# Kernel tuning notes

Hardware: AMD Instinct MI355X
Metric: run time of the kernel (lower is better)

## Reference

```python
import jax, jax.numpy as jnp
import numpy as np

TEMP = 0.1
EPS = 1e-9  # torch CosineSimilarity eps


def setup_inputs() -> dict:
    key = jax.random.key(0)
    k1, k2 = jax.random.split(key)
    h = jax.random.normal(k1, (16384, 2048), dtype=jnp.float32)
    W = jax.random.normal(k2, (512, 2048), dtype=jnp.float32) * (1.0 / np.sqrt(2048))
    return {"h": h, "W": W}


def reference(h, W):
    # process_reps: h already 2D -> identity. Split into anchor / context halves.
    B = h.shape[0] // 2
    wz = h[:B] @ W.T      # [B, low_rank_dim]
    wc = h[B:] @ W.T      # [B, low_rank_dim]

    # CosineSimilarity(dim=-1, eps=1e-9): dot / max(||z||*||c||, eps), pairwise BxB
    nz = jnp.linalg.norm(wz, axis=-1)  # [B]
    nc = jnp.linalg.norm(wc, axis=-1)  # [B]
    sim = (wz @ wc.T) / jnp.maximum(nz[:, None] * nc[None, :], EPS)  # [B, B]
    sim = sim / TEMP

    sim_mean = sim.mean()
    sim_pos = jnp.diagonal(sim).mean()
    logprob = -jax.nn.log_softmax(sim, axis=1)
    loss = jnp.diagonal(logprob).mean()
    # matches loss_dict entries: {'loss', 'loss_pos', 'loss_neg'}
    return jnp.stack([loss, sim_pos, sim_mean])
```

## Files before the change

kernel.cpp:

```cpp
#include <hip/hip_runtime.h>


typedef __attribute__((ext_vector_type(8))) short bf16x8;
typedef __attribute__((ext_vector_type(4))) float floatx4;
typedef unsigned char uchar;

__device__ __forceinline__ unsigned short f2bf(float f) {
    union { float f; unsigned u; } v; v.f = f;
    unsigned r = (v.u + 0x7FFFu + ((v.u >> 16) & 1u)) >> 16;
    return (unsigned short)r;
}

__device__ __forceinline__ void async_copy16(const void* g, void* l) {
    __builtin_amdgcn_global_load_lds(
        (const __attribute__((address_space(1))) void*)g,
        (__attribute__((address_space(3))) void*)l,
        16, 0, 0);
}

__global__ __launch_bounds__(256) void cast_fp8_kernel(
    const float* __restrict__ src, uchar* __restrict__ dst, int n, float scale)
{
    const int i = (blockIdx.x * 256 + threadIdx.x) * 8;
    if (i + 7 < n) {
        float4 a = *reinterpret_cast<const float4*>(src + i);
        float4 b = *reinterpret_cast<const float4*>(src + i + 4);
        const int p01 = __builtin_amdgcn_cvt_pk_fp8_f32(a.x * scale, a.y * scale, 0, 0);
        const int p23 = __builtin_amdgcn_cvt_pk_fp8_f32(a.z * scale, a.w * scale, 0, 0);
        const int p45 = __builtin_amdgcn_cvt_pk_fp8_f32(b.x * scale, b.y * scale, 0, 0);
        const int p67 = __builtin_amdgcn_cvt_pk_fp8_f32(b.z * scale, b.w * scale, 0, 0);
        int2 w;
        w.x = (p01 & 0xffff) | (p23 << 16);
        w.y = (p45 & 0xffff) | (p67 << 16);
        *reinterpret_cast<int2*>(dst + i) = w;
    }
}

__device__ __forceinline__ size_t fl_off(int row_g, int col_g) {
    const int g = row_g >> 4, r15 = row_g & 15;
    const int c = col_g >> 5, q = (col_g >> 3) & 3, b = col_g & 7;
    return ((size_t)g * 16 + c) * 512 + (size_t)(q * 16 + r15) * 8 + b;
}

__global__ __launch_bounds__(256) void g1_main(
    const uchar* __restrict__ h8, const uchar* __restrict__ W8,
    uchar* __restrict__ Z8F, float* __restrict__ norm2)
{
    __shared__ __align__(16) uchar As[128 * 64];
    __shared__ __align__(16) uchar Bs[128 * 64];

    const int bn = blockIdx.x;
    const int bm = blockIdx.y;
    const int t = threadIdx.x;
    const int wave = t >> 6, lane = t & 63;
    const int wm = wave & 1, wn = wave >> 1;
    const int quad = lane >> 4, l15 = lane & 15;

    floatx4 acc[4][4];
    #pragma unroll
    for (int i = 0; i < 4; i++)
        #pragma unroll
        for (int j = 0; j < 4; j++) acc[i][j] = {0.f, 0.f, 0.f, 0.f};

    const int srow0 = wave * 32 + (lane >> 2);
    const int srow1 = srow0 + 16;
    const int p = lane & 3;
    const int sw0 = (p ^ ((srow0 >> 1) & 3)) << 4;
    const int sw1 = (p ^ ((srow1 >> 1) & 3)) << 4;
    const uchar* gA0 = h8 + (size_t)(bm * 128 + srow0) * 2048 + sw0;
    const uchar* gA1 = h8 + (size_t)(bm * 128 + srow1) * 2048 + sw1;
    const uchar* gB0 = W8 + (size_t)(bn * 128 + srow0) * 2048 + sw0;
    const uchar* gB1 = W8 + (size_t)(bn * 128 + srow1) * 2048 + sw1;
    uchar* lA0 = &As[(wave * 32 +  0) * 64];
    uchar* lA1 = &As[(wave * 32 + 16) * 64];
    uchar* lB0 = &Bs[(wave * 32 +  0) * 64];
    uchar* lB1 = &Bs[(wave * 32 + 16) * 64];

    for (int k0 = 0; k0 < 2048; k0 += 64) {
        async_copy16(gA0 + k0, lA0);
        async_copy16(gA1 + k0, lA1);
        async_copy16(gB0 + k0, lB0);
        async_copy16(gB1 + k0, lB1);
        __syncthreads();
        #pragma unroll
        for (int ch = 0; ch < 2; ch++) {
            const int s = ch * 2 + (quad >> 1);
            const int sub = (quad & 1) * 8;
            long a[4], b[4];
            #pragma unroll
            for (int i = 0; i < 4; i++) {
                const int row = wm * 64 + i * 16 + l15;
                a[i] = *reinterpret_cast<const long*>(
                    &As[row * 64 + ((s ^ ((row >> 1) & 3)) << 4) + sub]);
            }
            #pragma unroll
            for (int j = 0; j < 4; j++) {
                const int row = wn * 64 + j * 16 + l15;
                b[j] = *reinterpret_cast<const long*>(
                    &Bs[row * 64 + ((s ^ ((row >> 1) & 3)) << 4) + sub]);
            }
            #pragma unroll
            for (int i = 0; i < 4; i++)
                #pragma unroll
                for (int j = 0; j < 4; j++)
                    acc[i][j] = __builtin_amdgcn_mfma_f32_16x16x32_fp8_fp8(
                        a[i], b[j], acc[i][j], 0, 0, 0);
        }
        __syncthreads();
    }

    #pragma unroll
    for (int i = 0; i < 4; i++) {
        #pragma unroll
        for (int r = 0; r < 4; r++) {
            const int row_g = bm * 128 + wm * 64 + i * 16 + quad * 4 + r;
            const int pk01 = __builtin_amdgcn_cvt_pk_fp8_f32(acc[i][0][r], acc[i][1][r], 0, 0);
            const int pk23 = __builtin_amdgcn_cvt_pk_fp8_f32(acc[i][2][r], acc[i][3][r], 0, 0);
            const uchar q8[4] = { (uchar)(pk01 & 0xff), (uchar)((pk01 >> 8) & 0xff),
                                  (uchar)(pk23 & 0xff), (uchar)((pk23 >> 8) & 0xff) };
            #pragma unroll
            for (int j = 0; j < 4; j++) {
                const int col_g = bn * 128 + wn * 64 + j * 16 + l15;
                Z8F[fl_off(row_g, col_g)] = q8[j];
            }
            const float q0 = __builtin_amdgcn_cvt_f32_fp8(pk01, 0);
            const float q1 = __builtin_amdgcn_cvt_f32_fp8(pk01, 1);
            const float q2 = __builtin_amdgcn_cvt_f32_fp8(pk23, 0);
            const float q3 = __builtin_amdgcn_cvt_f32_fp8(pk23, 1);
            float pw = q0 * q0 + q1 * q1 + q2 * q2 + q3 * q3;
            pw += __shfl_xor(pw, 1, 16);
            pw += __shfl_xor(pw, 2, 16);
            pw += __shfl_xor(pw, 4, 16);
            pw += __shfl_xor(pw, 8, 16);
            if (l15 == 0) atomicAdd(&norm2[row_g], pw);
        }
    }
}

__global__ __launch_bounds__(256) void g1_slow(
    const float* __restrict__ h, const float* __restrict__ W,
    uchar* __restrict__ Z8F, float* __restrict__ norm2)
{
    __shared__ __align__(16) unsigned short As[128][40];
    __shared__ __align__(16) unsigned short Bs[128][40];

    const int bn = blockIdx.x, bm = blockIdx.y;
    const int t = threadIdx.x;
    const int wave = t >> 6, lane = t & 63;
    const int wm = wave & 1, wn = wave >> 1;
    const int quad = lane >> 4, l15 = lane & 15;

    floatx4 acc[4][4];
    #pragma unroll
    for (int i = 0; i < 4; i++)
        #pragma unroll
        for (int j = 0; j < 4; j++) acc[i][j] = {0.f, 0.f, 0.f, 0.f};

    const int lrow = t >> 1, lhalf = t & 1;
    const float* ga = h + (size_t)(bm * 128 + lrow) * 2048 + lhalf * 16;
    const float* gb = W + (size_t)(bn * 128 + lrow) * 2048 + lhalf * 16;

    for (int k0 = 0; k0 < 2048; k0 += 32) {
        #pragma unroll
        for (int c = 0; c < 4; c++) {
            const float4 va = *reinterpret_cast<const float4*>(ga + k0 + c * 4);
            const float4 vb = *reinterpret_cast<const float4*>(gb + k0 + c * 4);
            ushort4 ua = make_ushort4(f2bf(va.x), f2bf(va.y), f2bf(va.z), f2bf(va.w));
            ushort4 ub = make_ushort4(f2bf(vb.x), f2bf(vb.y), f2bf(vb.z), f2bf(vb.w));
            *reinterpret_cast<ushort4*>(&As[lrow][lhalf * 16 + c * 4]) = ua;
            *reinterpret_cast<ushort4*>(&Bs[lrow][lhalf * 16 + c * 4]) = ub;
        }
        __syncthreads();
        bf16x8 af[4], bfr[4];
        #pragma unroll
        for (int i = 0; i < 4; i++)
            af[i] = *reinterpret_cast<const bf16x8*>(&As[wm * 64 + i * 16 + l15][quad * 8]);
        #pragma unroll
        for (int j = 0; j < 4; j++)
            bfr[j] = *reinterpret_cast<const bf16x8*>(&Bs[wn * 64 + j * 16 + l15][quad * 8]);
        #pragma unroll
        for (int i = 0; i < 4; i++)
            #pragma unroll
            for (int j = 0; j < 4; j++)
                acc[i][j] = __builtin_amdgcn_mfma_f32_16x16x32_bf16(af[i], bfr[j], acc[i][j], 0, 0, 0);
        __syncthreads();
    }

    #pragma unroll
    for (int i = 0; i < 4; i++) {
        #pragma unroll
        for (int r = 0; r < 4; r++) {
            const int row_g = bm * 128 + wm * 64 + i * 16 + quad * 4 + r;
            const int pk01 = __builtin_amdgcn_cvt_pk_fp8_f32(acc[i][0][r], acc[i][1][r], 0, 0);
            const int pk23 = __builtin_amdgcn_cvt_pk_fp8_f32(acc[i][2][r], acc[i][3][r], 0, 0);
            const uchar q8[4] = { (uchar)(pk01 & 0xff), (uchar)((pk01 >> 8) & 0xff),
                                  (uchar)(pk23 & 0xff), (uchar)((pk23 >> 8) & 0xff) };
            #pragma unroll
            for (int j = 0; j < 4; j++) {
                const int col_g = bn * 128 + wn * 64 + j * 16 + l15;
                Z8F[fl_off(row_g, col_g)] = q8[j];
            }
            const float q0 = __builtin_amdgcn_cvt_f32_fp8(pk01, 0);
            const float q1 = __builtin_amdgcn_cvt_f32_fp8(pk01, 1);
            const float q2 = __builtin_amdgcn_cvt_f32_fp8(pk23, 0);
            const float q3 = __builtin_amdgcn_cvt_f32_fp8(pk23, 1);
            float pw = q0 * q0 + q1 * q1 + q2 * q2 + q3 * q3;
            pw += __shfl_xor(pw, 1, 16);
            pw += __shfl_xor(pw, 2, 16);
            pw += __shfl_xor(pw, 4, 16);
            pw += __shfl_xor(pw, 8, 16);
            if (l15 == 0) atomicAdd(&norm2[row_g], pw);
        }
    }
}

__global__ __launch_bounds__(256, 2) void g2_main(
    const uchar* __restrict__ Z8F, const float* __restrict__ norm2,
    float* __restrict__ rowse, float* __restrict__ bsum, float* __restrict__ bdiag)
{
    __shared__ float lds_red[2][128][18];
    __shared__ float red[8];

    const int bn = blockIdx.x;
    const int bm = blockIdx.y;
    const int t = threadIdx.x;
    const int wave = t >> 6, lane = t & 63;
    const int wm = wave & 1, wn = wave >> 1;
    const int quad = lane >> 4, l15 = lane & 15;

    floatx4 acc[4][4];
    #pragma unroll
    for (int i = 0; i < 4; i++)
        #pragma unroll
        for (int j = 0; j < 4; j++) acc[i][j] = {0.f, 0.f, 0.f, 0.f};

    const uchar* baseA = Z8F + ((size_t)(bm * 8 + wm * 4) * 16) * 512 + lane * 8;
    const uchar* baseB = Z8F + ((size_t)(512 + bn * 8 + wn * 4) * 16) * 512 + lane * 8;

    #pragma unroll 4
    for (int c = 0; c < 16; c++) {
        long a[4], b[4];
        #pragma unroll
        for (int i = 0; i < 4; i++) {
            a[i] = *reinterpret_cast<const long*>(baseA + i * 8192 + c * 512);
            b[i] = *reinterpret_cast<const long*>(baseB + i * 8192 + c * 512);
        }
        #pragma unroll
        for (int i = 0; i < 4; i++)
            #pragma unroll
            for (int j = 0; j < 4; j++)
                acc[i][j] = __builtin_amdgcn_mfma_f32_16x16x32_fp8_fp8(a[i], b[j], acc[i][j], 0, 0, 0);
    }

    float rc4[4];
    #pragma unroll
    for (int j = 0; j < 4; j++)
        rc4[j] = rsqrtf(fmaxf(norm2[8192 + bn * 128 + wn * 64 + j * 16 + l15], 1e-30f));

    const bool diagblk = (bm == bn) && (wm == wn);
    float s_tot2 = 0.f, s_diag2 = 0.f;
    #pragma unroll
    for (int i = 0; i < 4; i++) {
        #pragma unroll
        for (int r = 0; r < 4; r++) {
            const int row_t = wm * 64 + i * 16 + quad * 4 + r;
            const float rzl2 = rsqrtf(fmaxf(norm2[bm * 128 + row_t], 1e-30f)) * 14.4269504089f;
            float rx = 0.f;
            #pragma unroll
            for (int j = 0; j < 4; j++) {
                const float sim2 = acc[i][j][r] * rzl2 * rc4[j];
                s_tot2 += sim2;
                rx += exp2f(sim2);
            }
            lds_red[wn][row_t][l15] = rx;
            if (diagblk) {
                const float sdv = acc[i][i][r] * rzl2 * rc4[i];
                s_diag2 += (l15 == quad * 4 + r) ? sdv : 0.f;
            }
        }
    }
    __syncthreads();

    {
        const int row_t = t >> 1, part = t & 1;
        float v = 0.f;
        #pragma unroll
        for (int c = 0; c < 16; c++) v += lds_red[part][row_t][c];
        v += __shfl_xor(v, 1, 64);
        if (part == 0) atomicAdd(&rowse[bm * 128 + row_t], v);
    }

    #pragma unroll
    for (int off = 32; off; off >>= 1) {
        s_tot2  += __shfl_xor(s_tot2, off, 64);
        s_diag2 += __shfl_xor(s_diag2, off, 64);
    }
    if (lane == 0) { red[wave] = s_tot2; red[4 + wave] = s_diag2; }
    __syncthreads();
    if (t == 0) {
        bsum[bm * 64 + bn]  = (red[0] + red[1] + red[2] + red[3]) * 0.69314718056f;
        bdiag[bm * 64 + bn] = (red[4] + red[5] + red[6] + red[7]) * 0.69314718056f;
    }
}

__global__ __launch_bounds__(256) void finalize_kernel(
    const float* __restrict__ rowse, const float* __restrict__ bsum,
    const float* __restrict__ bdiag, float* __restrict__ out)
{
    float a = 0.f, b = 0.f, c = 0.f;
    for (int i = threadIdx.x; i < 8192; i += 256) a += logf(rowse[i]);
    for (int i = threadIdx.x; i < 4096; i += 256) { b += bsum[i]; c += bdiag[i]; }
    #pragma unroll
    for (int off = 32; off; off >>= 1) {
        a += __shfl_xor(a, off, 64);
        b += __shfl_xor(b, off, 64);
        c += __shfl_xor(c, off, 64);
    }
    __shared__ float ra[4], rb[4], rc[4];
    const int wave = threadIdx.x >> 6, lane = threadIdx.x & 63;
    if (lane == 0) { ra[wave] = a; rb[wave] = b; rc[wave] = c; }
    __syncthreads();
    if (threadIdx.x == 0) {
        const float A = ra[0] + ra[1] + ra[2] + ra[3];
        const float B = rb[0] + rb[1] + rb[2] + rb[3];
        const float C = rc[0] + rc[1] + rc[2] + rc[3];
        const float diag_mean = C / 8192.f;
        out[0] = A / 8192.f - diag_mean;
        out[1] = diag_mean;
        out[2] = B / (8192.f * 8192.f);
    }
}

extern "C" void kernel_launch(void* const* d_in, const int* in_sizes, int n_in,
                              void* d_out, int out_size, void* d_ws, size_t ws_size,
                              hipStream_t stream) {
    const float* h = (const float*)d_in[0];
    const float* W = (const float*)d_in[1];
    float* out = (float*)d_out;

    char* ws = (char*)d_ws;
    float* norm2 = (float*)(ws);
    float* rowse = (float*)(ws + 65536);
    float* bsum  = (float*)(ws + 98304);
    float* bdiag = (float*)(ws + 114688);
    uchar* Z8F   = (uchar*)(ws + 131072);
    uchar* W8    = (uchar*)(ws + 8519680);
    uchar* h8    = (uchar*)(ws + 9568256);
    const size_t NEED_FAST = 43122688ull;

    hipMemsetAsync(ws, 0, 131072, stream);

    if (ws_size >= NEED_FAST) {
        const int nh = 16384 * 2048, nw = 512 * 2048;
        hipLaunchKernelGGL(cast_fp8_kernel, dim3(nh / 2048), dim3(256), 0, stream, h, h8, nh, 1.0f);
        hipLaunchKernelGGL(cast_fp8_kernel, dim3(nw / 2048), dim3(256), 0, stream, W, W8, nw, 32.0f);
        hipLaunchKernelGGL(g1_main, dim3(4, 128), dim3(256), 0, stream, h8, W8, Z8F, norm2);
    } else {
        hipLaunchKernelGGL(g1_slow, dim3(4, 128), dim3(256), 0, stream, h, W, Z8F, norm2);
    }
    hipLaunchKernelGGL(g2_main, dim3(64, 64), dim3(256), 0, stream, Z8F, norm2, rowse, bsum, bdiag);
    hipLaunchKernelGGL(finalize_kernel, dim3(1), dim3(256), 0, stream, rowse, bsum, bdiag, out);
}
```

Measured before the change: 329.7 us.

## Remap blocks per XCD for L2 reuse and software-pipeline fp8 MFMA loads

```diff
diff --git a/kernel.cpp b/kernel.cpp
--- a/kernel.cpp
+++ b/kernel.cpp
@@ -49,8 +49,10 @@
     __shared__ __align__(16) uchar As[128 * 64];
     __shared__ __align__(16) uchar Bs[128 * 64];
 
-    const int bn = blockIdx.x;
-    const int bm = blockIdx.y;
+    const int o = blockIdx.y * 4 + blockIdx.x;
+    const int xcd = o & 7, idx = o >> 3;
+    const int bn = idx & 3;
+    const int bm = xcd * 16 + (idx >> 2);
     const int t = threadIdx.x;
     const int wave = t >> 6, lane = t & 63;
     const int wm = wave & 1, wn = wave >> 1;
@@ -214,15 +216,18 @@
     }
 }
 
-__global__ __launch_bounds__(256, 2) void g2_main(
+__global__ __launch_bounds__(256, 4) void g2_main(
     const uchar* __restrict__ Z8F, const float* __restrict__ norm2,
     float* __restrict__ rowse, float* __restrict__ bsum, float* __restrict__ bdiag)
 {
-    __shared__ float lds_red[2][128][18];
+    __shared__ float lds_red[2][128][19];
     __shared__ float red[8];
 
-    const int bn = blockIdx.x;
-    const int bm = blockIdx.y;
+    const int o = blockIdx.y * 64 + blockIdx.x;
+    const int xcd = o & 7, idx = o >> 3;
+    const int bg = idx >> 7, r = idx & 127;
+    const int bm = xcd * 8 + (r >> 4);
+    const int bn = bg * 16 + (r & 15);
     const int t = threadIdx.x;
     const int wave = t >> 6, lane = t & 63;
     const int wm = wave & 1, wn = wave >> 1;
@@ -237,19 +242,30 @@
     const uchar* baseA = Z8F + ((size_t)(bm * 8 + wm * 4) * 16) * 512 + lane * 8;
     const uchar* baseB = Z8F + ((size_t)(512 + bn * 8 + wn * 4) * 16) * 512 + lane * 8;
 
-    #pragma unroll 4
+    long a[2][4], b[2][4];
+    #pragma unroll
+    for (int i = 0; i < 4; i++) {
+        a[0][i] = *reinterpret_cast<const long*>(baseA + i * 8192);
+        b[0][i] = *reinterpret_cast<const long*>(baseB + i * 8192);
+    }
+    #pragma unroll
     for (int c = 0; c < 16; c++) {
-        long a[4], b[4];
-        #pragma unroll
-        for (int i = 0; i < 4; i++) {
-            a[i] = *reinterpret_cast<const long*>(baseA + i * 8192 + c * 512);
-            b[i] = *reinterpret_cast<const long*>(baseB + i * 8192 + c * 512);
-        }
+        const int cur = c & 1, nxt = cur ^ 1;
+        if (c < 15) {
+            #pragma unroll
+            for (int i = 0; i < 4; i++) {
+                a[nxt][i] = *reinterpret_cast<const long*>(baseA + i * 8192 + (c + 1) * 512);
+                b[nxt][i] = *reinterpret_cast<const long*>(baseB + i * 8192 + (c + 1) * 512);
+            }
+        }
+        __builtin_amdgcn_s_setprio(1);
         #pragma unroll
         for (int i = 0; i < 4; i++)
             #pragma unroll
             for (int j = 0; j < 4; j++)
-                acc[i][j] = __builtin_amdgcn_mfma_f32_16x16x32_fp8_fp8(a[i], b[j], acc[i][j], 0, 0, 0);
+                acc[i][j] = __builtin_amdgcn_mfma_f32_16x16x32_fp8_fp8(
+                    a[cur][i], b[cur][j], acc[i][j], 0, 0, 0);
+        __builtin_amdgcn_s_setprio(0);
     }
 
     float rc4[4];
@@ -262,20 +278,20 @@
     #pragma unroll
     for (int i = 0; i < 4; i++) {
         #pragma unroll
-        for (int r = 0; r < 4; r++) {
-            const int row_t = wm * 64 + i * 16 + quad * 4 + r;
+        for (int rr = 0; rr < 4; rr++) {
+            const int row_t = wm * 64 + i * 16 + quad * 4 + rr;
             const float rzl2 = rsqrtf(fmaxf(norm2[bm * 128 + row_t], 1e-30f)) * 14.4269504089f;
             float rx = 0.f;
             #pragma unroll
             for (int j = 0; j < 4; j++) {
-                const float sim2 = acc[i][j][r] * rzl2 * rc4[j];
+                const float sim2 = acc[i][j][rr] * rzl2 * rc4[j];
                 s_tot2 += sim2;
                 rx += exp2f(sim2);
             }
             lds_red[wn][row_t][l15] = rx;
             if (diagblk) {
-                const float sdv = acc[i][i][r] * rzl2 * rc4[i];
-                s_diag2 += (l15 == quad * 4 + r) ? sdv : 0.f;
+                const float sdv = acc[i][i][rr] * rzl2 * rc4[i];
+                s_diag2 += (l15 == quad * 4 + rr) ? sdv : 0.f;
             }
         }
     }
```

Measured after the change: 316.5 us. 4.0% less time.
